# Performance work log

Hardware: AMD Instinct MI355X
Metric: run time of the kernel (lower is better)

## Reference

```python
import jax, jax.numpy as jnp
import numpy as np

B, NLEV, NX, NXSFC, NY, NYSFC, H, NHMEM = 4096, 60, 15, 24, 5, 5, 192, 16
G = 4 * H  # torch LSTM gate dim (i,f,g,o)


def setup_inputs() -> dict:
    key = jax.random.key(0)
    ks = jax.random.split(key, 32)
    rn = lambda k, s, sc=1.0: jax.random.normal(k, s, dtype=jnp.float32) * sc
    W = 0.05  # weight init scale for stability
    return {
        "x_lev": rn(ks[0], (B, NLEV, NX)),
        "x_sfc": rn(ks[1], (B, NXSFC)),
        "h_mem": jnp.zeros((B, NLEV, NHMEM), jnp.float32),
        "xmean_lev": rn(ks[2], (NLEV, NX), 0.1),
        "xdiv_lev": jax.random.uniform(ks[3], (NLEV, NX), dtype=jnp.float32) + 0.5,
        "xmean_sca": rn(ks[4], (NXSFC,), 0.1),
        "xdiv_sca": jax.random.uniform(ks[5], (NXSFC,), dtype=jnp.float32) + 0.5,
        "yscale_lev": jax.random.uniform(ks[6], (NLEV, NY), dtype=jnp.float32) + 0.5,
        "yscale_sca": jax.random.uniform(ks[7], (NY,), dtype=jnp.float32) + 0.5,
        "Wih1": rn(ks[8], (G, NX + NHMEM), W), "Whh1": rn(ks[9], (G, H), W), "b1": rn(ks[10], (G,), W),
        "Wih2": rn(ks[11], (G, H), W), "Whh2": rn(ks[12], (G, H), W), "b2": rn(ks[13], (G,), W),
        "Wsfc1": rn(ks[14], (H, NXSFC), W), "bsfc1": rn(ks[15], (H,), W),
        "Wsfc2": rn(ks[16], (H, NXSFC), W), "bsfc2": rn(ks[17], (H,), W),
        "Wtoa1": rn(ks[18], (H, 2), W), "btoa1": rn(ks[19], (H,), W),
        "Wtoa2": rn(ks[20], (H, 2), W), "btoa2": rn(ks[21], (H,), W),
        "Wlat": rn(ks[22], (NHMEM, H), W), "blat": rn(ks[23], (NHMEM,), W),
        "Wout": rn(ks[24], (NY, NHMEM), W), "bout": rn(ks[25], (NY,), W),
        "Wsfcout": rn(ks[26], (NY, H), W), "bsfcout": rn(ks[27], (NY,), W),
    }


def _lstm(x, h0, c0, Wih, Whh, b):
    """batch-first LSTM over the level dim. x: [B,L,nin]. Returns ([B,L,H], last h)."""
    xg = jnp.einsum('bli,gi->blg', x, Wih) + b  # precompute input projection
    def step(carry, xg_t):
        h, c = carry
        g = xg_t + h @ Whh.T
        i, f, gg, o = jnp.split(g, 4, axis=-1)  # torch gate order i,f,g,o
        c = jax.nn.sigmoid(f) * c + jax.nn.sigmoid(i) * jnp.tanh(gg)
        h = jax.nn.sigmoid(o) * jnp.tanh(c)
        return (h, c), h
    (hL, _), hs = jax.lax.scan(step, (h0, c0), jnp.swapaxes(xg, 0, 1))
    return jnp.swapaxes(hs, 0, 1), hL


def reference(x_lev, x_sfc, h_mem, xmean_lev, xdiv_lev, xmean_sca, xdiv_sca,
              yscale_lev, yscale_sca, Wih1, Whh1, b1, Wih2, Whh2, b2,
              Wsfc1, bsfc1, Wsfc2, bsfc2, Wtoa1, btoa1, Wtoa2, btoa2,
              Wlat, blat, Wout, bout, Wsfcout, bsfcout):
    # normalize
    xn = (x_lev - xmean_lev) / xdiv_lev                # [B,L,nx]
    sn = (x_sfc - xmean_sca) / xdiv_sca                # [B,nx_sfc]
    # surface MLPs initialize (h0, c0) of the upward LSTM
    h0 = jnp.tanh(sn @ Wsfc1.T + bsfc1)
    c0 = jnp.tanh(sn @ Wsfc2.T + bsfc2)
    # rnn1: concat latent memory to level inputs, scan surface -> TOA (flip levels)
    x1 = jnp.concatenate([xn, h_mem], axis=-1)[:, ::-1]
    hs1, _ = _lstm(x1, h0, c0, Wih1, Whh1, b1)
    hs1 = hs1[:, ::-1]                                  # back to TOA-first order
    # rnn2: TOA-initialized (2 solar scalars), scan TOA -> surface
    toa = sn[:, 0:2]
    h02 = jnp.tanh(toa @ Wtoa1.T + btoa1)
    c02 = jnp.tanh(toa @ Wtoa2.T + btoa2)
    hs2, h_last = _lstm(hs1, h02, c02, Wih2, Whh2, b2)
    # intermediate latent MLP -> new memory; output heads; denorm by yscale
    lat = hs2 @ Wlat.T + blat                           # [B,L,nh_mem]
    out = (lat @ Wout.T + bout) / yscale_lev            # [B,L,ny]
    out_sfc = (h_last @ Wsfcout.T + bsfcout) / yscale_sca  # [B,ny_sfc]
    return out, out_sfc, lat
```

## Files before the change

kernel.cpp:

```cpp
#include <hip/hip_runtime.h>
#include <hip/hip_bf16.h>


#define DEV static __device__ __forceinline__

typedef __attribute__((ext_vector_type(8))) short bf16x8;
typedef __attribute__((ext_vector_type(4))) float f32x4;

DEV unsigned short f2bf(float f) {
  unsigned int u = __builtin_bit_cast(unsigned int, f);
  unsigned int r = (u + 0x7fffu + ((u >> 16) & 1u)) >> 16;
  return (unsigned short)r;
}
DEV float bf2f(unsigned short s) {
  return __builtin_bit_cast(float, ((unsigned int)s) << 16);
}
DEV float sigm(float x) {
  float e = __builtin_amdgcn_exp2f(-1.44269504089f * x);
  return __builtin_amdgcn_rcpf(1.0f + e);
}
DEV float tanhf_(float x) {
  float e = __builtin_amdgcn_exp2f(2.88539008178f * x);
  return 1.0f - 2.0f * __builtin_amdgcn_rcpf(1.0f + e);
}

#define SEG_B2H 336
#define SEG_B2X 624
#define PACK_TOTAL (912 * 512)

#define HS1_OFF   1048576u
#define HS1_BYTES 94371840u
#define CWS_OFF   95420416u
#define CWS_BYTES 3145728u
#define XG2_OFF   98566144u
#define XG2_PER_LEVEL 12582912u
#define NEED_MIN  (HS1_OFF + HS1_BYTES)

__global__ void pack_kernel(const float* __restrict__ Wih1,
                            const float* __restrict__ Whh1,
                            const float* __restrict__ b1,
                            const float* __restrict__ Wih2,
                            const float* __restrict__ Whh2,
                            unsigned short* __restrict__ pw) {
  int idx = blockIdx.x * 256 + threadIdx.x;
  int j = idx & 7;
  int lane = (idx >> 3) & 63;
  int rest = idx >> 9;
  int n, k; float v;
  if (rest < SEG_B2H) {
    int kk = rest / 48, nt = rest % 48;
    n = nt * 16 + (lane & 15);
    k = kk * 32 + (lane >> 4) * 8 + j;
    if (k < 192) v = Whh1[n * 192 + k];
    else { int t = k - 192; v = (t < 31) ? Wih1[n * 31 + t] : b1[n]; }
  } else if (rest < SEG_B2X) {
    int r2 = rest - SEG_B2H; int kk = r2 / 48, nt = r2 % 48;
    n = nt * 16 + (lane & 15);
    k = kk * 32 + (lane >> 4) * 8 + j;
    v = Whh2[n * 192 + k];
  } else {
    int r2 = rest - SEG_B2X; int kk = r2 / 48, nt = r2 % 48;
    n = nt * 16 + (lane & 15);
    k = kk * 32 + (lane >> 4) * 8 + j;
    v = Wih2[n * 192 + k];
  }
  pw[idx] = f2bf(v);
}

__global__ __launch_bounds__(512, 2) void k1_lstm1(
    const float* __restrict__ xlev, const float* __restrict__ xsfc,
    const float* __restrict__ hmem,
    const float* __restrict__ xmean_lev, const float* __restrict__ xdiv_lev,
    const float* __restrict__ xmean_sca, const float* __restrict__ xdiv_sca,
    const float* __restrict__ Wsfc1, const float* __restrict__ bsfc1,
    const float* __restrict__ Wsfc2, const float* __restrict__ bsfc2,
    const unsigned short* __restrict__ pw,
    unsigned short* __restrict__ hs1g) {

  __shared__ float g_lds[16 * 772];
  __shared__ __align__(16) unsigned short a_lds[16 * 392];
  __shared__ float misc[16 * 24];

  const int tid = threadIdx.x;
  const int lane = tid & 63;
  const int wv = tid >> 6;
  const int bid = blockIdx.x;
  const int r0 = bid * 16;

  int erow[6], ecol[6];
  #pragma unroll
  for (int e = 0; e < 6; ++e) { int idx = tid + 512 * e; erow[e] = idx / 192; ecol[e] = idx % 192; }

  if (tid < 384) {
    int r = tid / 24, j = tid % 24;
    misc[tid] = (xsfc[(r0 + r) * 24 + j] - xmean_sca[j]) / xdiv_sca[j];
  }
  __syncthreads();

  float c[6];
  #pragma unroll
  for (int e = 0; e < 6; ++e) {
    int row = erow[e], col = ecol[e];
    float a1 = bsfc1[col], a2 = bsfc2[col];
    for (int k = 0; k < 24; ++k) {
      float s = misc[row * 24 + k];
      a1 = fmaf(s, Wsfc1[col * 24 + k], a1);
      a2 = fmaf(s, Wsfc2[col * 24 + k], a2);
    }
    a_lds[row * 392 + col] = f2bf(tanhf_(a1));
    c[e] = tanhf_(a2);
  }

  bf16x8 w1[7][6];
  #pragma unroll
  for (int kk = 0; kk < 7; ++kk)
    #pragma unroll
    for (int nt = 0; nt < 6; ++nt)
      w1[kk][nt] = *(const bf16x8*)&pw[((kk * 48 + wv * 6 + nt) * 64 + lane) * 8];

  const int xr = tid >> 5, xj = tid & 31;
  float xraw = 0.f;
  if (xj < 15)      xraw = __builtin_nontemporal_load(&xlev[((r0 + xr) * 60 + 59) * 15 + xj]);
  else if (xj < 31) xraw = __builtin_nontemporal_load(&hmem[((r0 + xr) * 60 + 59) * 16 + (xj - 15)]);

  for (int l = 59; l >= 0; --l) {
    {
      float v;
      if (xj < 15)      v = (xraw - xmean_lev[l * 15 + xj]) / xdiv_lev[l * 15 + xj];
      else if (xj < 31) v = xraw;
      else              v = 1.0f;
      a_lds[xr * 392 + 192 + xj] = f2bf(v);
    }
    if (l > 0) {
      if (xj < 15)      xraw = __builtin_nontemporal_load(&xlev[((r0 + xr) * 60 + l - 1) * 15 + xj]);
      else if (xj < 31) xraw = __builtin_nontemporal_load(&hmem[((r0 + xr) * 60 + l - 1) * 16 + (xj - 15)]);
    }
    __syncthreads();

    f32x4 acc[6];
    #pragma unroll
    for (int nt = 0; nt < 6; ++nt) acc[nt] = (f32x4){0.f, 0.f, 0.f, 0.f};
    #pragma unroll
    for (int kk = 0; kk < 7; ++kk) {
      const bf16x8 af = *(const bf16x8*)&a_lds[(lane & 15) * 392 + kk * 32 + (lane >> 4) * 8];
      #pragma unroll
      for (int nt = 0; nt < 6; ++nt)
        acc[nt] = __builtin_amdgcn_mfma_f32_16x16x32_bf16(af, w1[kk][nt], acc[nt], 0, 0, 0);
    }
    #pragma unroll
    for (int nt = 0; nt < 6; ++nt)
      #pragma unroll
      for (int q = 0; q < 4; ++q)
        g_lds[((lane >> 4) * 4 + q) * 772 + wv * 96 + nt * 16 + (lane & 15)] = acc[nt][q];
    __syncthreads();

    #pragma unroll
    for (int e = 0; e < 6; ++e) {
      int row = erow[e], col = ecol[e];
      float gi = g_lds[row * 772 + col];
      float gf = g_lds[row * 772 + 192 + col];
      float gg = g_lds[row * 772 + 384 + col];
      float go = g_lds[row * 772 + 576 + col];
      c[e] = sigm(gf) * c[e] + sigm(gi) * tanhf_(gg);
      float hv = sigm(go) * tanhf_(c[e]);
      unsigned short hb = f2bf(hv);
      a_lds[row * 392 + col] = hb;
      hs1g[(size_t)(bid * 60 + l) * 3072 + tid + 512 * e] = hb;
    }
  }
}

__global__ __launch_bounds__(512, 2) void k2_xg2(
    const unsigned short* __restrict__ pw,
    const unsigned short* __restrict__ hs1g,
    const float* __restrict__ b2,
    float* __restrict__ xg2, int l0, int Cc) {

  __shared__ __align__(16) unsigned short a2[8 * 16 * 200];

  const int tid = threadIdx.x;
  const int lane = tid & 63;
  const int wv = tid >> 6;
  const int g = blockIdx.x;

  bf16x8 wb[6][6];
  #pragma unroll
  for (int kk = 0; kk < 6; ++kk)
    #pragma unroll
    for (int nt = 0; nt < 6; ++nt)
      wb[kk][nt] = *(const bf16x8*)&pw[((SEG_B2X + kk * 48 + wv * 6 + nt) * 64 + lane) * 8];

  float b2v[6];
  #pragma unroll
  for (int nt = 0; nt < 6; ++nt) b2v[nt] = b2[wv * 96 + nt * 16 + (lane & 15)];

  #pragma unroll
  for (int i = 0; i < 6; ++i) {
    int flat16 = tid + 512 * i;
    int sub = flat16 / 384, within = flat16 % 384;
    int p2 = g * 8 + sub;
    int b3 = p2 / Cc, dl = p2 % Cc;
    bf16x8 v = *(const bf16x8*)&hs1g[(size_t)(b3 * 60 + l0 + dl) * 3072 + within * 8];
    int row = within / 24, col = (within % 24) * 8;
    *(bf16x8*)&a2[(sub * 16 + row) * 200 + col] = v;
  }
  __syncthreads();

  f32x4* xv = (f32x4*)xg2;
  for (int sub = 0; sub < 8; ++sub) {
    f32x4 acc[6];
    #pragma unroll
    for (int nt = 0; nt < 6; ++nt)
      acc[nt] = (f32x4){b2v[nt], b2v[nt], b2v[nt], b2v[nt]};
    #pragma unroll
    for (int kk = 0; kk < 6; ++kk) {
      const bf16x8 af = *(const bf16x8*)&a2[(sub * 16 + (lane & 15)) * 200 + kk * 32 + (lane >> 4) * 8];
      #pragma unroll
      for (int nt = 0; nt < 6; ++nt)
        acc[nt] = __builtin_amdgcn_mfma_f32_16x16x32_bf16(af, wb[kk][nt], acc[nt], 0, 0, 0);
    }
    int p2 = g * 8 + sub;
    #pragma unroll
    for (int nt = 0; nt < 6; ++nt)
      xv[(size_t)((p2 * 8 + wv) * 6 + nt) * 64 + lane] = acc[nt];
  }
}

__global__ __launch_bounds__(512, 2) void k3_lstm2(
    const float* __restrict__ xsfc,
    const float* __restrict__ xmean_sca, const float* __restrict__ xdiv_sca,
    const float* __restrict__ Wtoa1, const float* __restrict__ btoa1,
    const float* __restrict__ Wtoa2, const float* __restrict__ btoa2,
    const unsigned short* __restrict__ pw,
    const float* __restrict__ xg2,
    unsigned short* __restrict__ hs2,
    float* __restrict__ cws,
    int l0, int l1, int savec) {

  __shared__ float g_lds[16 * 772];
  __shared__ __align__(16) unsigned short a_lds[16 * 392];

  const int tid = threadIdx.x;
  const int lane = tid & 63;
  const int wv = tid >> 6;
  const int bid = blockIdx.x;
  const int r0 = bid * 16;
  const int Cc = l1 - l0;

  int erow[6], ecol[6];
  #pragma unroll
  for (int e = 0; e < 6; ++e) { int idx = tid + 512 * e; erow[e] = idx / 192; ecol[e] = idx % 192; }

  float c[6];
  if (l0 == 0) {
    #pragma unroll
    for (int e = 0; e < 6; ++e) {
      int row = erow[e], col = ecol[e];
      float t0 = (xsfc[(r0 + row) * 24 + 0] - xmean_sca[0]) / xdiv_sca[0];
      float t1 = (xsfc[(r0 + row) * 24 + 1] - xmean_sca[1]) / xdiv_sca[1];
      float a1 = fmaf(t0, Wtoa1[col * 2], fmaf(t1, Wtoa1[col * 2 + 1], btoa1[col]));
      float a2 = fmaf(t0, Wtoa2[col * 2], fmaf(t1, Wtoa2[col * 2 + 1], btoa2[col]));
      a_lds[row * 392 + col] = f2bf(tanhf_(a1));
      c[e] = tanhf_(a2);
    }
  } else {
    #pragma unroll
    for (int e = 0; e < 6; ++e) {
      a_lds[erow[e] * 392 + ecol[e]] = hs2[(size_t)(bid * 60 + (l0 - 1)) * 3072 + tid + 512 * e];
      c[e] = cws[bid * 3072 + tid + 512 * e];
    }
  }

  bf16x8 w2[6][6];
  #pragma unroll
  for (int kk = 0; kk < 6; ++kk)
    #pragma unroll
    for (int nt = 0; nt < 6; ++nt)
      w2[kk][nt] = *(const bf16x8*)&pw[((SEG_B2H + kk * 48 + wv * 6 + nt) * 64 + lane) * 8];

  const f32x4* xv = (const f32x4*)xg2;
  f32x4 cur[6];
  #pragma unroll
  for (int nt = 0; nt < 6; ++nt)
    cur[nt] = xv[(size_t)((bid * Cc + 0) * 8 + wv) * 6 * 64 + nt * 64 + lane];
  __syncthreads();

  for (int l = l0; l < l1; ++l) {
    f32x4 nxt[6];
    if (l + 1 < l1) {
      int p2n = bid * Cc + (l + 1 - l0);
      #pragma unroll
      for (int nt = 0; nt < 6; ++nt)
        nxt[nt] = xv[(size_t)(p2n * 8 + wv) * 6 * 64 + nt * 64 + lane];
    }

    f32x4 acc[6];
    #pragma unroll
    for (int nt = 0; nt < 6; ++nt) acc[nt] = cur[nt];
    #pragma unroll
    for (int kk = 0; kk < 6; ++kk) {
      const bf16x8 af = *(const bf16x8*)&a_lds[(lane & 15) * 392 + kk * 32 + (lane >> 4) * 8];
      #pragma unroll
      for (int nt = 0; nt < 6; ++nt)
        acc[nt] = __builtin_amdgcn_mfma_f32_16x16x32_bf16(af, w2[kk][nt], acc[nt], 0, 0, 0);
    }
    #pragma unroll
    for (int nt = 0; nt < 6; ++nt)
      #pragma unroll
      for (int q = 0; q < 4; ++q)
        g_lds[((lane >> 4) * 4 + q) * 772 + wv * 96 + nt * 16 + (lane & 15)] = acc[nt][q];
    __syncthreads();

    #pragma unroll
    for (int e = 0; e < 6; ++e) {
      int row = erow[e], col = ecol[e];
      float gi = g_lds[row * 772 + col];
      float gf = g_lds[row * 772 + 192 + col];
      float gg = g_lds[row * 772 + 384 + col];
      float go = g_lds[row * 772 + 576 + col];
      c[e] = sigm(gf) * c[e] + sigm(gi) * tanhf_(gg);
      unsigned short hb = f2bf(sigm(go) * tanhf_(c[e]));
      a_lds[row * 392 + col] = hb;
      hs2[(size_t)(bid * 60 + l) * 3072 + tid + 512 * e] = hb;
    }
    if (l + 1 < l1) {
      #pragma unroll
      for (int nt = 0; nt < 6; ++nt) cur[nt] = nxt[nt];
    }
    __syncthreads();
  }

  if (savec) {
    #pragma unroll
    for (int e = 0; e < 6; ++e)
      cws[bid * 3072 + tid + 512 * e] = c[e];
  }
}

__global__ __launch_bounds__(256, 4) void k4_out(
    const unsigned short* __restrict__ hs2,
    const float* __restrict__ Wlat, const float* __restrict__ blat,
    const float* __restrict__ Wout, const float* __restrict__ bout,
    const float* __restrict__ Wsfcout, const float* __restrict__ bsfcout,
    const float* __restrict__ yscale_lev, const float* __restrict__ yscale_sca,
    float* __restrict__ out, float* __restrict__ outsfc, float* __restrict__ latout) {

  __shared__ float wl[16 * 192];
  const int tid = threadIdx.x;
  const int bid = blockIdx.x;

  if (bid < 960) {
    for (int i = tid; i < 3072; i += 256) wl[i] = Wlat[i];
    __syncthreads();
    int R = bid * 256 + tid;
    int b = R / 60, l = R % 60, b3 = b >> 4, r = b & 15;
    const unsigned short* hp = hs2 + (size_t)(b3 * 60 + l) * 3072 + r * 192;
    float lat[16];
    #pragma unroll
    for (int cc = 0; cc < 16; ++cc) lat[cc] = blat[cc];
    for (int k8 = 0; k8 < 24; ++k8) {
      bf16x8 hv = *(const bf16x8*)&hp[k8 * 8];
      #pragma unroll
      for (int j = 0; j < 8; ++j) {
        float hf = bf2f((unsigned short)hv[j]);
        #pragma unroll
        for (int cc = 0; cc < 16; ++cc) lat[cc] = fmaf(hf, wl[cc * 192 + k8 * 8 + j], lat[cc]);
      }
    }
    #pragma unroll
    for (int cc = 0; cc < 16; ++cc)
      latout[(size_t)R * 16 + cc] = lat[cc];
    #pragma unroll
    for (int y = 0; y < 5; ++y) {
      float ov = bout[y];
      #pragma unroll
      for (int cc = 0; cc < 16; ++cc) ov = fmaf(lat[cc], Wout[y * 16 + cc], ov);
      out[(size_t)R * 5 + y] = ov / yscale_lev[l * 5 + y];
    }
  } else {
    for (int i = tid; i < 960; i += 256) wl[i] = Wsfcout[i];
    __syncthreads();
    int r = (bid - 960) * 256 + tid;
    int b3 = r >> 4, rr = r & 15;
    const unsigned short* hp = hs2 + (size_t)(b3 * 60 + 59) * 3072 + rr * 192;
    float a5[5];
    #pragma unroll
    for (int y = 0; y < 5; ++y) a5[y] = bsfcout[y];
    for (int k8 = 0; k8 < 24; ++k8) {
      bf16x8 hv = *(const bf16x8*)&hp[k8 * 8];
      #pragma unroll
      for (int j = 0; j < 8; ++j) {
        float hf = bf2f((unsigned short)hv[j]);
        #pragma unroll
        for (int y = 0; y < 5; ++y) a5[y] = fmaf(hf, wl[y * 192 + k8 * 8 + j], a5[y]);
      }
    }
    #pragma unroll
    for (int y = 0; y < 5; ++y)
      outsfc[(size_t)r * 5 + y] = a5[y] / yscale_sca[y];
  }
}

__global__ __launch_bounds__(512, 2) void lstm_main(
    const float* __restrict__ xlev, const float* __restrict__ xsfc,
    const float* __restrict__ hmem,
    const float* __restrict__ xmean_lev, const float* __restrict__ xdiv_lev,
    const float* __restrict__ xmean_sca, const float* __restrict__ xdiv_sca,
    const float* __restrict__ yscale_lev, const float* __restrict__ yscale_sca,
    const float* __restrict__ b2,
    const float* __restrict__ Wsfc1, const float* __restrict__ bsfc1,
    const float* __restrict__ Wsfc2, const float* __restrict__ bsfc2,
    const float* __restrict__ Wtoa1, const float* __restrict__ btoa1,
    const float* __restrict__ Wtoa2, const float* __restrict__ btoa2,
    const float* __restrict__ Wlat, const float* __restrict__ blat,
    const float* __restrict__ Wout, const float* __restrict__ bout,
    const float* __restrict__ Wsfcout, const float* __restrict__ bsfcout,
    const unsigned short* __restrict__ pw,
    unsigned short* __restrict__ hs1g,
    float* __restrict__ out, float* __restrict__ outsfc, float* __restrict__ latout) {

  __shared__ float g_lds[16 * 772];
  __shared__ __align__(16) unsigned short a_lds[16 * 392];
  __shared__ float misc[16 * 24];
  __shared__ float toa_lds[32];

  const int tid = threadIdx.x;
  const int lane = tid & 63;
  const int wv = tid >> 6;
  const int bid = blockIdx.x;
  const int r0 = bid * 16;

  int erow[6], ecol[6];
  #pragma unroll
  for (int e = 0; e < 6; ++e) { int idx = tid + 512 * e; erow[e] = idx / 192; ecol[e] = idx % 192; }

  if (tid < 384) {
    int r = tid / 24, j = tid % 24;
    misc[tid] = (xsfc[(r0 + r) * 24 + j] - xmean_sca[j]) / xdiv_sca[j];
  }
  __syncthreads();
  if (tid < 32) toa_lds[tid] = misc[(tid >> 1) * 24 + (tid & 1)];

  float c[6];
  #pragma unroll
  for (int e = 0; e < 6; ++e) {
    int row = erow[e], col = ecol[e];
    float a1 = bsfc1[col], a2 = bsfc2[col];
    for (int k = 0; k < 24; ++k) {
      float s = misc[row * 24 + k];
      a1 = fmaf(s, Wsfc1[col * 24 + k], a1);
      a2 = fmaf(s, Wsfc2[col * 24 + k], a2);
    }
    a_lds[row * 392 + col] = f2bf(tanhf_(a1));
    c[e] = tanhf_(a2);
  }

  bf16x8 w1[7][6];
  #pragma unroll
  for (int kk = 0; kk < 7; ++kk)
    #pragma unroll
    for (int nt = 0; nt < 6; ++nt)
      w1[kk][nt] = *(const bf16x8*)&pw[((kk * 48 + wv * 6 + nt) * 64 + lane) * 8];

  const int xr = tid >> 5, xj = tid & 31;
  float xraw = 0.f;
  if (xj < 15)      xraw = __builtin_nontemporal_load(&xlev[((r0 + xr) * 60 + 59) * 15 + xj]);
  else if (xj < 31) xraw = __builtin_nontemporal_load(&hmem[((r0 + xr) * 60 + 59) * 16 + (xj - 15)]);

  for (int l = 59; l >= 0; --l) {
    {
      float v;
      if (xj < 15)      v = (xraw - xmean_lev[l * 15 + xj]) / xdiv_lev[l * 15 + xj];
      else if (xj < 31) v = xraw;
      else              v = 1.0f;
      a_lds[xr * 392 + 192 + xj] = f2bf(v);
    }
    if (l > 0) {
      if (xj < 15)      xraw = __builtin_nontemporal_load(&xlev[((r0 + xr) * 60 + l - 1) * 15 + xj]);
      else if (xj < 31) xraw = __builtin_nontemporal_load(&hmem[((r0 + xr) * 60 + l - 1) * 16 + (xj - 15)]);
    }
    __syncthreads();

    f32x4 acc[6];
    #pragma unroll
    for (int nt = 0; nt < 6; ++nt) acc[nt] = (f32x4){0.f, 0.f, 0.f, 0.f};
    #pragma unroll
    for (int kk = 0; kk < 7; ++kk) {
      const bf16x8 af = *(const bf16x8*)&a_lds[(lane & 15) * 392 + kk * 32 + (lane >> 4) * 8];
      #pragma unroll
      for (int nt = 0; nt < 6; ++nt)
        acc[nt] = __builtin_amdgcn_mfma_f32_16x16x32_bf16(af, w1[kk][nt], acc[nt], 0, 0, 0);
    }
    #pragma unroll
    for (int nt = 0; nt < 6; ++nt)
      #pragma unroll
      for (int q = 0; q < 4; ++q)
        g_lds[((lane >> 4) * 4 + q) * 772 + wv * 96 + nt * 16 + (lane & 15)] = acc[nt][q];
    __syncthreads();

    #pragma unroll
    for (int e = 0; e < 6; ++e) {
      int row = erow[e], col = ecol[e];
      float gi = g_lds[row * 772 + col];
      float gf = g_lds[row * 772 + 192 + col];
      float gg = g_lds[row * 772 + 384 + col];
      float go = g_lds[row * 772 + 576 + col];
      c[e] = sigm(gf) * c[e] + sigm(gi) * tanhf_(gg);
      float hv = sigm(go) * tanhf_(c[e]);
      unsigned short hb = f2bf(hv);
      a_lds[row * 392 + col] = hb;
      __builtin_nontemporal_store(hb, &hs1g[(bid * 60 + l) * 3072 + tid + 512 * e]);
    }
  }

  #pragma unroll
  for (int e = 0; e < 6; ++e) {
    int row = erow[e], col = ecol[e];
    float t0 = toa_lds[row * 2], t1 = toa_lds[row * 2 + 1];
    float a1 = fmaf(t0, Wtoa1[col * 2], fmaf(t1, Wtoa1[col * 2 + 1], btoa1[col]));
    float a2 = fmaf(t0, Wtoa2[col * 2], fmaf(t1, Wtoa2[col * 2 + 1], btoa2[col]));
    a_lds[row * 392 + col] = f2bf(tanhf_(a1));
    c[e] = tanhf_(a2);
  }
  bf16x8 w2[6][6];
  #pragma unroll
  for (int kk = 0; kk < 6; ++kk)
    #pragma unroll
    for (int nt = 0; nt < 6; ++nt)
      w2[kk][nt] = *(const bf16x8*)&pw[((SEG_B2H + kk * 48 + wv * 6 + nt) * 64 + lane) * 8];

  const bf16x8* hs1v = (const bf16x8*)hs1g;
  bf16x8 hv8;
  if (tid < 384) hv8 = __builtin_nontemporal_load(&hs1v[(bid * 60 + 0) * 384 + tid]);

  for (int l = 0; l < 60; ++l) {
    if (tid < 384)
      *(bf16x8*)&a_lds[(tid / 24) * 392 + 192 + (tid % 24) * 8] = hv8;
    if (tid < 384 && l < 59)
      hv8 = __builtin_nontemporal_load(&hs1v[(bid * 60 + l + 1) * 384 + tid]);

    bf16x8 wx0[6], wx1[6];
    #pragma unroll
    for (int nt = 0; nt < 6; ++nt)
      wx0[nt] = *(const bf16x8*)&pw[((SEG_B2X + 0 * 48 + wv * 6 + nt) * 64 + lane) * 8];
    #pragma unroll
    for (int nt = 0; nt < 6; ++nt)
      wx1[nt] = *(const bf16x8*)&pw[((SEG_B2X + 1 * 48 + wv * 6 + nt) * 64 + lane) * 8];

    __syncthreads();

    f32x4 acc[6];
    #pragma unroll
    for (int nt = 0; nt < 6; ++nt) acc[nt] = (f32x4){0.f, 0.f, 0.f, 0.f};

    #pragma unroll
    for (int g = 0; g < 6; ++g) {
      const bf16x8 ah = *(const bf16x8*)&a_lds[(lane & 15) * 392 + g * 32 + (lane >> 4) * 8];
      #pragma unroll
      for (int nt = 0; nt < 6; ++nt)
        acc[nt] = __builtin_amdgcn_mfma_f32_16x16x32_bf16(ah, w2[g][nt], acc[nt], 0, 0, 0);
      const bf16x8 ax = *(const bf16x8*)&a_lds[(lane & 15) * 392 + 192 + g * 32 + (lane >> 4) * 8];
      #pragma unroll
      for (int nt = 0; nt < 6; ++nt)
        acc[nt] = __builtin_amdgcn_mfma_f32_16x16x32_bf16(ax, (g & 1) ? wx1[nt] : wx0[nt], acc[nt], 0, 0, 0);
      if (g < 4) {
        #pragma unroll
        for (int nt = 0; nt < 6; ++nt) {
          bf16x8 nw = *(const bf16x8*)&pw[((SEG_B2X + (g + 2) * 48 + wv * 6 + nt) * 64 + lane) * 8];
          if (g & 1) wx1[nt] = nw; else wx0[nt] = nw;
        }
      }
    }
    #pragma unroll
    for (int nt = 0; nt < 6; ++nt)
      #pragma unroll
      for (int q = 0; q < 4; ++q)
        g_lds[((lane >> 4) * 4 + q) * 772 + wv * 96 + nt * 16 + (lane & 15)] = acc[nt][q];
    __syncthreads();

    #pragma unroll
    for (int e = 0; e < 6; ++e) {
      int row = erow[e], col = ecol[e];
      float gi = g_lds[row * 772 + col]       + b2[col];
      float gf = g_lds[row * 772 + 192 + col] + b2[192 + col];
      float gg = g_lds[row * 772 + 384 + col] + b2[384 + col];
      float go = g_lds[row * 772 + 576 + col] + b2[576 + col];
      c[e] = sigm(gf) * c[e] + sigm(gi) * tanhf_(gg);
      a_lds[row * 392 + col] = f2bf(sigm(go) * tanhf_(c[e]));
    }
    __syncthreads();

    if (tid < 256) {
      int r = tid >> 4, cc = tid & 15;
      float lv = blat[cc];
      for (int k = 0; k < 192; k += 8) {
        #pragma unroll
        for (int jj = 0; jj < 8; ++jj)
          lv = fmaf(bf2f(a_lds[r * 392 + k + jj]), Wlat[cc * 192 + k + jj], lv);
      }
      __builtin_nontemporal_store(lv, &latout[((r0 + r) * 60 + l) * 16 + cc]);
      misc[r * 16 + cc] = lv;
    }
    __syncthreads();
    if (tid < 80) {
      int r = tid / 5, y = tid % 5;
      float ov = bout[y];
      #pragma unroll
      for (int k = 0; k < 16; ++k) ov = fmaf(misc[r * 16 + k], Wout[y * 16 + k], ov);
      __builtin_nontemporal_store(ov / yscale_lev[l * 5 + y], &out[((r0 + r) * 60 + l) * 5 + y]);
    }
  }

  if (tid < 80) {
    int r = tid / 5, y = tid % 5;
    float ov = bsfcout[y];
    for (int k = 0; k < 192; ++k)
      ov = fmaf(bf2f(a_lds[r * 392 + k]), Wsfcout[y * 192 + k], ov);
    outsfc[(r0 + r) * 5 + y] = ov / yscale_sca[y];
  }
}

extern "C" void kernel_launch(void* const* d_in, const int* in_sizes, int n_in,
                              void* d_out, int out_size, void* d_ws, size_t ws_size,
                              hipStream_t stream) {
  (void)in_sizes; (void)n_in; (void)out_size;

  const float* xlev      = (const float*)d_in[0];
  const float* xsfc      = (const float*)d_in[1];
  const float* hmem      = (const float*)d_in[2];
  const float* xmean_lev = (const float*)d_in[3];
  const float* xdiv_lev  = (const float*)d_in[4];
  const float* xmean_sca = (const float*)d_in[5];
  const float* xdiv_sca  = (const float*)d_in[6];
  const float* yscale_lev= (const float*)d_in[7];
  const float* yscale_sca= (const float*)d_in[8];
  const float* Wih1      = (const float*)d_in[9];
  const float* Whh1      = (const float*)d_in[10];
  const float* b1        = (const float*)d_in[11];
  const float* Wih2      = (const float*)d_in[12];
  const float* Whh2      = (const float*)d_in[13];
  const float* b2        = (const float*)d_in[14];
  const float* Wsfc1     = (const float*)d_in[15];
  const float* bsfc1     = (const float*)d_in[16];
  const float* Wsfc2     = (const float*)d_in[17];
  const float* bsfc2     = (const float*)d_in[18];
  const float* Wtoa1     = (const float*)d_in[19];
  const float* btoa1     = (const float*)d_in[20];
  const float* Wtoa2     = (const float*)d_in[21];
  const float* btoa2     = (const float*)d_in[22];
  const float* Wlat      = (const float*)d_in[23];
  const float* blat      = (const float*)d_in[24];
  const float* Wout      = (const float*)d_in[25];
  const float* bout      = (const float*)d_in[26];
  const float* Wsfcout   = (const float*)d_in[27];
  const float* bsfcout   = (const float*)d_in[28];

  unsigned short* pw   = (unsigned short*)d_ws;
  unsigned short* hsg  = (unsigned short*)((char*)d_ws + HS1_OFF);
  float* cws           = (float*)((char*)d_ws + CWS_OFF);
  float* xg2           = (float*)((char*)d_ws + XG2_OFF);
  float* out    = (float*)d_out;
  float* outsfc = out + (size_t)4096 * 60 * 5;
  float* latout = outsfc + (size_t)4096 * 5;

  long long avail = (long long)ws_size - (long long)XG2_OFF;
  int C = (avail > 0) ? (int)(avail / (long long)XG2_PER_LEVEL) : 0;
  if (C > 60) C = 60;

  hipLaunchKernelGGL(pack_kernel, dim3(PACK_TOTAL / 256), dim3(256), 0, stream,
                     Wih1, Whh1, b1, Wih2, Whh2, pw);

  if (C >= 1) {
    hipLaunchKernelGGL(k1_lstm1, dim3(256), dim3(512), 0, stream,
                       xlev, xsfc, hmem, xmean_lev, xdiv_lev, xmean_sca, xdiv_sca,
                       Wsfc1, bsfc1, Wsfc2, bsfc2, pw, hsg);
    int l0 = 0;
    while (l0 < 60) {
      int Cc = (60 - l0 < C) ? (60 - l0) : C;
      hipLaunchKernelGGL(k2_xg2, dim3(32 * Cc), dim3(512), 0, stream,
                         pw, hsg, b2, xg2, l0, Cc);
      hipLaunchKernelGGL(k3_lstm2, dim3(256), dim3(512), 0, stream,
                         xsfc, xmean_sca, xdiv_sca, Wtoa1, btoa1, Wtoa2, btoa2,
                         pw, xg2, hsg, cws, l0, l0 + Cc, (l0 + Cc < 60) ? 1 : 0);
      l0 += Cc;
    }
    hipLaunchKernelGGL(k4_out, dim3(976), dim3(256), 0, stream,
                       hsg, Wlat, blat, Wout, bout, Wsfcout, bsfcout,
                       yscale_lev, yscale_sca, out, outsfc, latout);
  } else if (ws_size >= (size_t)NEED_MIN) {
    hipLaunchKernelGGL(lstm_main, dim3(256), dim3(512), 0, stream,
                       xlev, xsfc, hmem, xmean_lev, xdiv_lev, xmean_sca, xdiv_sca,
                       yscale_lev, yscale_sca, b2,
                       Wsfc1, bsfc1, Wsfc2, bsfc2, Wtoa1, btoa1, Wtoa2, btoa2,
                       Wlat, blat, Wout, bout, Wsfcout, bsfcout,
                       pw, hsg, out, outsfc, latout);
  }
}
```

Measured before the change: 777.8 us.

## Fuse both LSTM scans and the Wih2 projection into one persistent kernel

Merges the LSTM1 scan, the chunked LSTM2 input projection and the LSTM2 scan into a single templated kernel launched once per batch tile. Each block computes its own chunk of `xg2` with MFMA, writes it to global memory, then runs the recurrent steps for that chunk, so the cell state stays in registers between chunks. This removes the per-chunk launches and the c-state save and restore through memory. In exchange, the projection now runs serially inside the 256 recurrent blocks instead of on a wider grid. The larger shared-memory footprint and the `accG[CC][6]` register array risk lower occupancy and register spills.

```diff
diff --git a/kernel.cpp b/kernel.cpp
--- a/kernel.cpp
+++ b/kernel.cpp
@@ -28,13 +28,11 @@
 #define SEG_B2X 624
 #define PACK_TOTAL (912 * 512)
 
-#define HS1_OFF   1048576u
-#define HS1_BYTES 94371840u
-#define CWS_OFF   95420416u
-#define CWS_BYTES 3145728u
-#define XG2_OFF   98566144u
+#define HS_OFF    1048576u
+#define HS_BYTES  94371840u
+#define XG2_OFF   95420416u
 #define XG2_PER_LEVEL 12582912u
-#define NEED_MIN  (HS1_OFF + HS1_BYTES)
+#define NEED_MIN  (HS_OFF + HS_BYTES)
 
 __global__ void pack_kernel(const float* __restrict__ Wih1,
                             const float* __restrict__ Whh1,
@@ -67,18 +65,24 @@
   pw[idx] = f2bf(v);
 }
 
-__global__ __launch_bounds__(512, 2) void k1_lstm1(
+template <int CC>
+__global__ __launch_bounds__(512, 2) void mono(
     const float* __restrict__ xlev, const float* __restrict__ xsfc,
     const float* __restrict__ hmem,
     const float* __restrict__ xmean_lev, const float* __restrict__ xdiv_lev,
     const float* __restrict__ xmean_sca, const float* __restrict__ xdiv_sca,
     const float* __restrict__ Wsfc1, const float* __restrict__ bsfc1,
     const float* __restrict__ Wsfc2, const float* __restrict__ bsfc2,
+    const float* __restrict__ Wtoa1, const float* __restrict__ btoa1,
+    const float* __restrict__ Wtoa2, const float* __restrict__ btoa2,
+    const float* __restrict__ b2,
     const unsigned short* __restrict__ pw,
-    unsigned short* __restrict__ hs1g) {
+    unsigned short* __restrict__ hsg,
+    float* __restrict__ xg2) {
 
   __shared__ float g_lds[16 * 772];
   __shared__ __align__(16) unsigned short a_lds[16 * 392];
+  __shared__ __align__(16) unsigned short a2[CC * 16 * 200];
   __shared__ float misc[16 * 24];
 
   const int tid = threadIdx.x;
@@ -101,239 +105,197 @@
   #pragma unroll
   for (int e = 0; e < 6; ++e) {
     int row = erow[e], col = ecol[e];
-    float a1 = bsfc1[col], a2 = bsfc2[col];
+    float a1 = bsfc1[col], a2v = bsfc2[col];
     for (int k = 0; k < 24; ++k) {
       float s = misc[row * 24 + k];
-      a1 = fmaf(s, Wsfc1[col * 24 + k], a1);
-      a2 = fmaf(s, Wsfc2[col * 24 + k], a2);
+      a1  = fmaf(s, Wsfc1[col * 24 + k], a1);
+      a2v = fmaf(s, Wsfc2[col * 24 + k], a2v);
     }
     a_lds[row * 392 + col] = f2bf(tanhf_(a1));
-    c[e] = tanhf_(a2);
-  }
-
-  bf16x8 w1[7][6];
-  #pragma unroll
-  for (int kk = 0; kk < 7; ++kk)
-    #pragma unroll
-    for (int nt = 0; nt < 6; ++nt)
-      w1[kk][nt] = *(const bf16x8*)&pw[((kk * 48 + wv * 6 + nt) * 64 + lane) * 8];
-
-  const int xr = tid >> 5, xj = tid & 31;
-  float xraw = 0.f;
-  if (xj < 15)      xraw = __builtin_nontemporal_load(&xlev[((r0 + xr) * 60 + 59) * 15 + xj]);
-  else if (xj < 31) xraw = __builtin_nontemporal_load(&hmem[((r0 + xr) * 60 + 59) * 16 + (xj - 15)]);
-
-  for (int l = 59; l >= 0; --l) {
+    c[e] = tanhf_(a2v);
+  }
+
+  {
+    bf16x8 w1[7][6];
+    #pragma unroll
+    for (int kk = 0; kk < 7; ++kk)
+      #pragma unroll
+      for (int nt = 0; nt < 6; ++nt)
+        w1[kk][nt] = *(const bf16x8*)&pw[((kk * 48 + wv * 6 + nt) * 64 + lane) * 8];
+
+    const int xr = tid >> 5, xj = tid & 31;
+    float xraw = 0.f;
+    if (xj < 15)      xraw = __builtin_nontemporal_load(&xlev[((r0 + xr) * 60 + 59) * 15 + xj]);
+    else if (xj < 31) xraw = __builtin_nontemporal_load(&hmem[((r0 + xr) * 60 + 59) * 16 + (xj - 15)]);
+
+    for (int l = 59; l >= 0; --l) {
+      {
+        float v;
+        if (xj < 15)      v = (xraw - xmean_lev[l * 15 + xj]) / xdiv_lev[l * 15 + xj];
+        else if (xj < 31) v = xraw;
+        else              v = 1.0f;
+        a_lds[xr * 392 + 192 + xj] = f2bf(v);
+      }
+      if (l > 0) {
+        if (xj < 15)      xraw = __builtin_nontemporal_load(&xlev[((r0 + xr) * 60 + l - 1) * 15 + xj]);
+        else if (xj < 31) xraw = __builtin_nontemporal_load(&hmem[((r0 + xr) * 60 + l - 1) * 16 + (xj - 15)]);
+      }
+      __syncthreads();
+
+      f32x4 acc[6];
+      #pragma unroll
+      for (int nt = 0; nt < 6; ++nt) acc[nt] = (f32x4){0.f, 0.f, 0.f, 0.f};
+      #pragma unroll
+      for (int kk = 0; kk < 7; ++kk) {
+        const bf16x8 af = *(const bf16x8*)&a_lds[(lane & 15) * 392 + kk * 32 + (lane >> 4) * 8];
+        #pragma unroll
+        for (int nt = 0; nt < 6; ++nt)
+          acc[nt] = __builtin_amdgcn_mfma_f32_16x16x32_bf16(af, w1[kk][nt], acc[nt], 0, 0, 0);
+      }
+      #pragma unroll
+      for (int nt = 0; nt < 6; ++nt)
+        #pragma unroll
+        for (int q = 0; q < 4; ++q)
+          g_lds[((lane >> 4) * 4 + q) * 772 + wv * 96 + nt * 16 + (lane & 15)] = acc[nt][q];
+      __syncthreads();
+
+      #pragma unroll
+      for (int e = 0; e < 6; ++e) {
+        int row = erow[e], col = ecol[e];
+        float gi = g_lds[row * 772 + col];
+        float gf = g_lds[row * 772 + 192 + col];
+        float gg = g_lds[row * 772 + 384 + col];
+        float go = g_lds[row * 772 + 576 + col];
+        c[e] = sigm(gf) * c[e] + sigm(gi) * tanhf_(gg);
+        float hv = sigm(go) * tanhf_(c[e]);
+        unsigned short hb = f2bf(hv);
+        a_lds[row * 392 + col] = hb;
+        hsg[(size_t)(bid * 60 + l) * 3072 + tid + 512 * e] = hb;
+      }
+    }
+  }
+
+  #pragma unroll
+  for (int e = 0; e < 6; ++e) {
+    int row = erow[e], col = ecol[e];
+    float t0 = (xsfc[(r0 + row) * 24 + 0] - xmean_sca[0]) / xdiv_sca[0];
+    float t1 = (xsfc[(r0 + row) * 24 + 1] - xmean_sca[1]) / xdiv_sca[1];
+    float a1 = fmaf(t0, Wtoa1[col * 2], fmaf(t1, Wtoa1[col * 2 + 1], btoa1[col]));
+    float a2v = fmaf(t0, Wtoa2[col * 2], fmaf(t1, Wtoa2[col * 2 + 1], btoa2[col]));
+    a_lds[row * 392 + col] = f2bf(tanhf_(a1));
+    c[e] = tanhf_(a2v);
+  }
+
+  float b2v[6];
+  #pragma unroll
+  for (int nt = 0; nt < 6; ++nt) b2v[nt] = b2[wv * 96 + nt * 16 + (lane & 15)];
+
+  f32x4* xv = (f32x4*)xg2;
+
+  for (int l0 = 0; l0 < 60; l0 += CC) {
+    __syncthreads();
+
+    #pragma unroll
+    for (int i = 0; i < (384 * CC + 511) / 512; ++i) {
+      int idx = tid + 512 * i;
+      if (idx < 384 * CC) {
+        int dl = idx / 384, within = idx % 384;
+        bf16x8 v = *(const bf16x8*)&hsg[(size_t)(bid * 60 + l0 + dl) * 3072 + within * 8];
+        *(bf16x8*)&a2[(dl * 16 + within / 24) * 200 + (within % 24) * 8] = v;
+      }
+    }
+    __syncthreads();
+
     {
-      float v;
-      if (xj < 15)      v = (xraw - xmean_lev[l * 15 + xj]) / xdiv_lev[l * 15 + xj];
-      else if (xj < 31) v = xraw;
-      else              v = 1.0f;
-      a_lds[xr * 392 + 192 + xj] = f2bf(v);
-    }
-    if (l > 0) {
-      if (xj < 15)      xraw = __builtin_nontemporal_load(&xlev[((r0 + xr) * 60 + l - 1) * 15 + xj]);
-      else if (xj < 31) xraw = __builtin_nontemporal_load(&hmem[((r0 + xr) * 60 + l - 1) * 16 + (xj - 15)]);
-    }
-    __syncthreads();
-
-    f32x4 acc[6];
-    #pragma unroll
-    for (int nt = 0; nt < 6; ++nt) acc[nt] = (f32x4){0.f, 0.f, 0.f, 0.f};
-    #pragma unroll
-    for (int kk = 0; kk < 7; ++kk) {
-      const bf16x8 af = *(const bf16x8*)&a_lds[(lane & 15) * 392 + kk * 32 + (lane >> 4) * 8];
-      #pragma unroll
-      for (int nt = 0; nt < 6; ++nt)
-        acc[nt] = __builtin_amdgcn_mfma_f32_16x16x32_bf16(af, w1[kk][nt], acc[nt], 0, 0, 0);
-    }
-    #pragma unroll
-    for (int nt = 0; nt < 6; ++nt)
-      #pragma unroll
-      for (int q = 0; q < 4; ++q)
-        g_lds[((lane >> 4) * 4 + q) * 772 + wv * 96 + nt * 16 + (lane & 15)] = acc[nt][q];
-    __syncthreads();
-
-    #pragma unroll
-    for (int e = 0; e < 6; ++e) {
-      int row = erow[e], col = ecol[e];
-      float gi = g_lds[row * 772 + col];
-      float gf = g_lds[row * 772 + 192 + col];
-      float gg = g_lds[row * 772 + 384 + col];
-      float go = g_lds[row * 772 + 576 + col];
-      c[e] = sigm(gf) * c[e] + sigm(gi) * tanhf_(gg);
-      float hv = sigm(go) * tanhf_(c[e]);
-      unsigned short hb = f2bf(hv);
-      a_lds[row * 392 + col] = hb;
-      hs1g[(size_t)(bid * 60 + l) * 3072 + tid + 512 * e] = hb;
-    }
-  }
-}
-
-__global__ __launch_bounds__(512, 2) void k2_xg2(
-    const unsigned short* __restrict__ pw,
-    const unsigned short* __restrict__ hs1g,
-    const float* __restrict__ b2,
-    float* __restrict__ xg2, int l0, int Cc) {
-
-  __shared__ __align__(16) unsigned short a2[8 * 16 * 200];
-
-  const int tid = threadIdx.x;
-  const int lane = tid & 63;
-  const int wv = tid >> 6;
-  const int g = blockIdx.x;
-
-  bf16x8 wb[6][6];
-  #pragma unroll
-  for (int kk = 0; kk < 6; ++kk)
-    #pragma unroll
-    for (int nt = 0; nt < 6; ++nt)
-      wb[kk][nt] = *(const bf16x8*)&pw[((SEG_B2X + kk * 48 + wv * 6 + nt) * 64 + lane) * 8];
-
-  float b2v[6];
-  #pragma unroll
-  for (int nt = 0; nt < 6; ++nt) b2v[nt] = b2[wv * 96 + nt * 16 + (lane & 15)];
-
-  #pragma unroll
-  for (int i = 0; i < 6; ++i) {
-    int flat16 = tid + 512 * i;
-    int sub = flat16 / 384, within = flat16 % 384;
-    int p2 = g * 8 + sub;
-    int b3 = p2 / Cc, dl = p2 % Cc;
-    bf16x8 v = *(const bf16x8*)&hs1g[(size_t)(b3 * 60 + l0 + dl) * 3072 + within * 8];
-    int row = within / 24, col = (within % 24) * 8;
-    *(bf16x8*)&a2[(sub * 16 + row) * 200 + col] = v;
-  }
-  __syncthreads();
-
-  f32x4* xv = (f32x4*)xg2;
-  for (int sub = 0; sub < 8; ++sub) {
-    f32x4 acc[6];
-    #pragma unroll
-    for (int nt = 0; nt < 6; ++nt)
-      acc[nt] = (f32x4){b2v[nt], b2v[nt], b2v[nt], b2v[nt]};
-    #pragma unroll
-    for (int kk = 0; kk < 6; ++kk) {
-      const bf16x8 af = *(const bf16x8*)&a2[(sub * 16 + (lane & 15)) * 200 + kk * 32 + (lane >> 4) * 8];
-      #pragma unroll
-      for (int nt = 0; nt < 6; ++nt)
-        acc[nt] = __builtin_amdgcn_mfma_f32_16x16x32_bf16(af, wb[kk][nt], acc[nt], 0, 0, 0);
-    }
-    int p2 = g * 8 + sub;
-    #pragma unroll
-    for (int nt = 0; nt < 6; ++nt)
-      xv[(size_t)((p2 * 8 + wv) * 6 + nt) * 64 + lane] = acc[nt];
-  }
-}
-
-__global__ __launch_bounds__(512, 2) void k3_lstm2(
-    const float* __restrict__ xsfc,
-    const float* __restrict__ xmean_sca, const float* __restrict__ xdiv_sca,
-    const float* __restrict__ Wtoa1, const float* __restrict__ btoa1,
-    const float* __restrict__ Wtoa2, const float* __restrict__ btoa2,
-    const unsigned short* __restrict__ pw,
-    const float* __restrict__ xg2,
-    unsigned short* __restrict__ hs2,
-    float* __restrict__ cws,
-    int l0, int l1, int savec) {
-
-  __shared__ float g_lds[16 * 772];
-  __shared__ __align__(16) unsigned short a_lds[16 * 392];
-
-  const int tid = threadIdx.x;
-  const int lane = tid & 63;
-  const int wv = tid >> 6;
-  const int bid = blockIdx.x;
-  const int r0 = bid * 16;
-  const int Cc = l1 - l0;
-
-  int erow[6], ecol[6];
-  #pragma unroll
-  for (int e = 0; e < 6; ++e) { int idx = tid + 512 * e; erow[e] = idx / 192; ecol[e] = idx % 192; }
-
-  float c[6];
-  if (l0 == 0) {
-    #pragma unroll
-    for (int e = 0; e < 6; ++e) {
-      int row = erow[e], col = ecol[e];
-      float t0 = (xsfc[(r0 + row) * 24 + 0] - xmean_sca[0]) / xdiv_sca[0];
-      float t1 = (xsfc[(r0 + row) * 24 + 1] - xmean_sca[1]) / xdiv_sca[1];
-      float a1 = fmaf(t0, Wtoa1[col * 2], fmaf(t1, Wtoa1[col * 2 + 1], btoa1[col]));
-      float a2 = fmaf(t0, Wtoa2[col * 2], fmaf(t1, Wtoa2[col * 2 + 1], btoa2[col]));
-      a_lds[row * 392 + col] = f2bf(tanhf_(a1));
-      c[e] = tanhf_(a2);
-    }
-  } else {
-    #pragma unroll
-    for (int e = 0; e < 6; ++e) {
-      a_lds[erow[e] * 392 + ecol[e]] = hs2[(size_t)(bid * 60 + (l0 - 1)) * 3072 + tid + 512 * e];
-      c[e] = cws[bid * 3072 + tid + 512 * e];
-    }
-  }
-
-  bf16x8 w2[6][6];
-  #pragma unroll
-  for (int kk = 0; kk < 6; ++kk)
-    #pragma unroll
-    for (int nt = 0; nt < 6; ++nt)
-      w2[kk][nt] = *(const bf16x8*)&pw[((SEG_B2H + kk * 48 + wv * 6 + nt) * 64 + lane) * 8];
-
-  const f32x4* xv = (const f32x4*)xg2;
-  f32x4 cur[6];
-  #pragma unroll
-  for (int nt = 0; nt < 6; ++nt)
-    cur[nt] = xv[(size_t)((bid * Cc + 0) * 8 + wv) * 6 * 64 + nt * 64 + lane];
-  __syncthreads();
-
-  for (int l = l0; l < l1; ++l) {
-    f32x4 nxt[6];
-    if (l + 1 < l1) {
-      int p2n = bid * Cc + (l + 1 - l0);
-      #pragma unroll
-      for (int nt = 0; nt < 6; ++nt)
-        nxt[nt] = xv[(size_t)(p2n * 8 + wv) * 6 * 64 + nt * 64 + lane];
-    }
-
-    f32x4 acc[6];
-    #pragma unroll
-    for (int nt = 0; nt < 6; ++nt) acc[nt] = cur[nt];
-    #pragma unroll
-    for (int kk = 0; kk < 6; ++kk) {
-      const bf16x8 af = *(const bf16x8*)&a_lds[(lane & 15) * 392 + kk * 32 + (lane >> 4) * 8];
-      #pragma unroll
-      for (int nt = 0; nt < 6; ++nt)
-        acc[nt] = __builtin_amdgcn_mfma_f32_16x16x32_bf16(af, w2[kk][nt], acc[nt], 0, 0, 0);
-    }
-    #pragma unroll
-    for (int nt = 0; nt < 6; ++nt)
-      #pragma unroll
-      for (int q = 0; q < 4; ++q)
-        g_lds[((lane >> 4) * 4 + q) * 772 + wv * 96 + nt * 16 + (lane & 15)] = acc[nt][q];
-    __syncthreads();
-
-    #pragma unroll
-    for (int e = 0; e < 6; ++e) {
-      int row = erow[e], col = ecol[e];
-      float gi = g_lds[row * 772 + col];
-      float gf = g_lds[row * 772 + 192 + col];
-      float gg = g_lds[row * 772 + 384 + col];
-      float go = g_lds[row * 772 + 576 + col];
-      c[e] = sigm(gf) * c[e] + sigm(gi) * tanhf_(gg);
-      unsigned short hb = f2bf(sigm(go) * tanhf_(c[e]));
-      a_lds[row * 392 + col] = hb;
-      hs2[(size_t)(bid * 60 + l) * 3072 + tid + 512 * e] = hb;
-    }
-    if (l + 1 < l1) {
-      #pragma unroll
-      for (int nt = 0; nt < 6; ++nt) cur[nt] = nxt[nt];
-    }
-    __syncthreads();
-  }
-
-  if (savec) {
-    #pragma unroll
-    for (int e = 0; e < 6; ++e)
-      cws[bid * 3072 + tid + 512 * e] = c[e];
+      f32x4 accG[CC][6];
+      #pragma unroll
+      for (int dl = 0; dl < CC; ++dl)
+        #pragma unroll
+        for (int nt = 0; nt < 6; ++nt)
+          accG[dl][nt] = (f32x4){b2v[nt], b2v[nt], b2v[nt], b2v[nt]};
+
+      bf16x8 wxA[6], wxB[6];
+      #pragma unroll
+      for (int nt = 0; nt < 6; ++nt)
+        wxA[nt] = *(const bf16x8*)&pw[((SEG_B2X + 0 * 48 + wv * 6 + nt) * 64 + lane) * 8];
+      #pragma unroll
+      for (int nt = 0; nt < 6; ++nt)
+        wxB[nt] = *(const bf16x8*)&pw[((SEG_B2X + 1 * 48 + wv * 6 + nt) * 64 + lane) * 8];
+
+      #pragma unroll
+      for (int kk = 0; kk < 6; ++kk) {
+        #pragma unroll
+        for (int dl = 0; dl < CC; ++dl) {
+          const bf16x8 af = *(const bf16x8*)&a2[(dl * 16 + (lane & 15)) * 200 + kk * 32 + (lane >> 4) * 8];
+          #pragma unroll
+          for (int nt = 0; nt < 6; ++nt)
+            accG[dl][nt] = __builtin_amdgcn_mfma_f32_16x16x32_bf16(
+                af, (kk & 1) ? wxB[nt] : wxA[nt], accG[dl][nt], 0, 0, 0);
+        }
+        if (kk < 4) {
+          #pragma unroll
+          for (int nt = 0; nt < 6; ++nt) {
+            bf16x8 nw = *(const bf16x8*)&pw[((SEG_B2X + (kk + 2) * 48 + wv * 6 + nt) * 64 + lane) * 8];
+            if (kk & 1) wxB[nt] = nw; else wxA[nt] = nw;
+          }
+        }
+      }
+
+      #pragma unroll
+      for (int dl = 0; dl < CC; ++dl)
+        #pragma unroll
+        for (int nt = 0; nt < 6; ++nt)
+          xv[(size_t)(((bid * CC + dl) * 8 + wv) * 6 + nt) * 64 + lane] = accG[dl][nt];
+    }
+    __syncthreads();
+
+    bf16x8 w2[6][6];
+    #pragma unroll
+    for (int kk = 0; kk < 6; ++kk)
+      #pragma unroll
+      for (int nt = 0; nt < 6; ++nt)
+        w2[kk][nt] = *(const bf16x8*)&pw[((SEG_B2H + kk * 48 + wv * 6 + nt) * 64 + lane) * 8];
+
+    #pragma unroll
+    for (int dl = 0; dl < CC; ++dl) {
+      const int l = l0 + dl;
+      f32x4 cur[6];
+      #pragma unroll
+      for (int nt = 0; nt < 6; ++nt)
+        cur[nt] = xv[(size_t)(((bid * CC + dl) * 8 + wv) * 6 + nt) * 64 + lane];
+
+      f32x4 acc[6];
+      #pragma unroll
+      for (int nt = 0; nt < 6; ++nt) acc[nt] = (f32x4){0.f, 0.f, 0.f, 0.f};
+      #pragma unroll
+      for (int kk = 0; kk < 6; ++kk) {
+        const bf16x8 af = *(const bf16x8*)&a_lds[(lane & 15) * 392 + kk * 32 + (lane >> 4) * 8];
+        #pragma unroll
+        for (int nt = 0; nt < 6; ++nt)
+          acc[nt] = __builtin_amdgcn_mfma_f32_16x16x32_bf16(af, w2[kk][nt], acc[nt], 0, 0, 0);
+      }
+      #pragma unroll
+      for (int nt = 0; nt < 6; ++nt)
+        #pragma unroll
+        for (int q = 0; q < 4; ++q)
+          g_lds[((lane >> 4) * 4 + q) * 772 + wv * 96 + nt * 16 + (lane & 15)] =
+              acc[nt][q] + cur[nt][q];
+      __syncthreads();
+
+      #pragma unroll
+      for (int e = 0; e < 6; ++e) {
+        int row = erow[e], col = ecol[e];
+        float gi = g_lds[row * 772 + col];
+        float gf = g_lds[row * 772 + 192 + col];
+        float gg = g_lds[row * 772 + 384 + col];
+        float go = g_lds[row * 772 + 576 + col];
+        c[e] = sigm(gf) * c[e] + sigm(gi) * tanhf_(gg);
+        unsigned short hb = f2bf(sigm(go) * tanhf_(c[e]));
+        a_lds[row * 392 + col] = hb;
+        hsg[(size_t)(bid * 60 + l) * 3072 + tid + 512 * e] = hb;
+      }
+      __syncthreads();
+    }
   }
 }
 
@@ -655,35 +617,31 @@
   const float* Wsfcout   = (const float*)d_in[27];
   const float* bsfcout   = (const float*)d_in[28];
 
-  unsigned short* pw   = (unsigned short*)d_ws;
-  unsigned short* hsg  = (unsigned short*)((char*)d_ws + HS1_OFF);
-  float* cws           = (float*)((char*)d_ws + CWS_OFF);
-  float* xg2           = (float*)((char*)d_ws + XG2_OFF);
+  unsigned short* pw  = (unsigned short*)d_ws;
+  unsigned short* hsg = (unsigned short*)((char*)d_ws + HS_OFF);
+  float* xg2          = (float*)((char*)d_ws + XG2_OFF);
   float* out    = (float*)d_out;
   float* outsfc = out + (size_t)4096 * 60 * 5;
   float* latout = outsfc + (size_t)4096 * 5;
 
-  long long avail = (long long)ws_size - (long long)XG2_OFF;
-  int C = (avail > 0) ? (int)(avail / (long long)XG2_PER_LEVEL) : 0;
-  if (C > 60) C = 60;
-
   hipLaunchKernelGGL(pack_kernel, dim3(PACK_TOTAL / 256), dim3(256), 0, stream,
                      Wih1, Whh1, b1, Wih2, Whh2, pw);
 
-  if (C >= 1) {
-    hipLaunchKernelGGL(k1_lstm1, dim3(256), dim3(512), 0, stream,
-                       xlev, xsfc, hmem, xmean_lev, xdiv_lev, xmean_sca, xdiv_sca,
-                       Wsfc1, bsfc1, Wsfc2, bsfc2, pw, hsg);
-    int l0 = 0;
-    while (l0 < 60) {
-      int Cc = (60 - l0 < C) ? (60 - l0) : C;
-      hipLaunchKernelGGL(k2_xg2, dim3(32 * Cc), dim3(512), 0, stream,
-                         pw, hsg, b2, xg2, l0, Cc);
-      hipLaunchKernelGGL(k3_lstm2, dim3(256), dim3(512), 0, stream,
-                         xsfc, xmean_sca, xdiv_sca, Wtoa1, btoa1, Wtoa2, btoa2,
-                         pw, xg2, hsg, cws, l0, l0 + Cc, (l0 + Cc < 60) ? 1 : 0);
-      l0 += Cc;
-    }
+  const size_t need6 = (size_t)XG2_OFF + 6ull * XG2_PER_LEVEL;
+  const size_t need3 = (size_t)XG2_OFF + 3ull * XG2_PER_LEVEL;
+  const size_t need1 = (size_t)XG2_OFF + 1ull * XG2_PER_LEVEL;
+
+  if (ws_size >= need1) {
+    #define MONO_ARGS xlev, xsfc, hmem, xmean_lev, xdiv_lev, xmean_sca, xdiv_sca, \
+                      Wsfc1, bsfc1, Wsfc2, bsfc2, Wtoa1, btoa1, Wtoa2, btoa2, b2, \
+                      pw, hsg, xg2
+    if (ws_size >= need6)
+      hipLaunchKernelGGL(mono<6>, dim3(256), dim3(512), 0, stream, MONO_ARGS);
+    else if (ws_size >= need3)
+      hipLaunchKernelGGL(mono<3>, dim3(256), dim3(512), 0, stream, MONO_ARGS);
+    else
+      hipLaunchKernelGGL(mono<1>, dim3(256), dim3(512), 0, stream, MONO_ARGS);
+    #undef MONO_ARGS
     hipLaunchKernelGGL(k4_out, dim3(976), dim3(256), 0, stream,
                        hsg, Wlat, blat, Wout, bout, Wsfcout, bsfcout,
                        yscale_lev, yscale_sca, out, outsfc, latout);
```

Result: slower. 1.275 ms (+64.0%).

## Use lighter LDS-only barriers, shrink xg2 tiles and add xg2 after MFMA

Applied to the files above, without the earlier changes.

Replaces __syncthreads with a custom barrier that waits only on LDS/scalar counters (lgkmcnt) before s_barrier, so outstanding global prefetch loads no longer stall each recurrence step. The xg2 projection kernel now does 2 sub-tiles per block instead of 8, with four times as many blocks, which cuts LDS use and adds parallelism at the cost of reloading the weight registers more often. In lstm2 the prefetched input projection is added at the LDS store instead of seeding the MFMA accumulator, which frees the MFMA chain from waiting on the global load. The custom barrier relies on global loads not being needed before the barrier, which holds only if no global writes are read across it.

```diff
diff --git a/kernel.cpp b/kernel.cpp
--- a/kernel.cpp
+++ b/kernel.cpp
@@ -23,18 +23,20 @@
   float e = __builtin_amdgcn_exp2f(2.88539008178f * x);
   return 1.0f - 2.0f * __builtin_amdgcn_rcpf(1.0f + e);
 }
+DEV void sbar() {
+  asm volatile("s_waitcnt lgkmcnt(0)\n\ts_barrier" ::: "memory");
+}
 
 #define SEG_B2H 336
 #define SEG_B2X 624
 #define PACK_TOTAL (912 * 512)
 
-#define HS1_OFF   1048576u
-#define HS1_BYTES 94371840u
+#define HS_OFF    1048576u
+#define HS_BYTES  94371840u
 #define CWS_OFF   95420416u
-#define CWS_BYTES 3145728u
 #define XG2_OFF   98566144u
 #define XG2_PER_LEVEL 12582912u
-#define NEED_MIN  (HS1_OFF + HS1_BYTES)
+#define NEED_MIN  (HS_OFF + HS_BYTES)
 
 __global__ void pack_kernel(const float* __restrict__ Wih1,
                             const float* __restrict__ Whh1,
@@ -135,7 +137,7 @@
       if (xj < 15)      xraw = __builtin_nontemporal_load(&xlev[((r0 + xr) * 60 + l - 1) * 15 + xj]);
       else if (xj < 31) xraw = __builtin_nontemporal_load(&hmem[((r0 + xr) * 60 + l - 1) * 16 + (xj - 15)]);
     }
-    __syncthreads();
+    sbar();
 
     f32x4 acc[6];
     #pragma unroll
@@ -152,7 +154,7 @@
       #pragma unroll
       for (int q = 0; q < 4; ++q)
         g_lds[((lane >> 4) * 4 + q) * 772 + wv * 96 + nt * 16 + (lane & 15)] = acc[nt][q];
-    __syncthreads();
+    sbar();
 
     #pragma unroll
     for (int e = 0; e < 6; ++e) {
@@ -176,7 +178,7 @@
     const float* __restrict__ b2,
     float* __restrict__ xg2, int l0, int Cc) {
 
-  __shared__ __align__(16) unsigned short a2[8 * 16 * 200];
+  __shared__ __align__(16) unsigned short a2[2 * 16 * 200];
 
   const int tid = threadIdx.x;
   const int lane = tid & 63;
@@ -195,19 +197,21 @@
   for (int nt = 0; nt < 6; ++nt) b2v[nt] = b2[wv * 96 + nt * 16 + (lane & 15)];
 
   #pragma unroll
-  for (int i = 0; i < 6; ++i) {
+  for (int i = 0; i < 2; ++i) {
     int flat16 = tid + 512 * i;
-    int sub = flat16 / 384, within = flat16 % 384;
-    int p2 = g * 8 + sub;
-    int b3 = p2 / Cc, dl = p2 % Cc;
-    bf16x8 v = *(const bf16x8*)&hs1g[(size_t)(b3 * 60 + l0 + dl) * 3072 + within * 8];
-    int row = within / 24, col = (within % 24) * 8;
-    *(bf16x8*)&a2[(sub * 16 + row) * 200 + col] = v;
-  }
-  __syncthreads();
+    if (flat16 < 768) {
+      int sub = flat16 / 384, within = flat16 % 384;
+      int p2 = g * 2 + sub;
+      int b3 = p2 / Cc, dl = p2 % Cc;
+      bf16x8 v = *(const bf16x8*)&hs1g[(size_t)(b3 * 60 + l0 + dl) * 3072 + within * 8];
+      *(bf16x8*)&a2[(sub * 16 + within / 24) * 200 + (within % 24) * 8] = v;
+    }
+  }
+  sbar();
 
   f32x4* xv = (f32x4*)xg2;
-  for (int sub = 0; sub < 8; ++sub) {
+  #pragma unroll
+  for (int sub = 0; sub < 2; ++sub) {
     f32x4 acc[6];
     #pragma unroll
     for (int nt = 0; nt < 6; ++nt)
@@ -219,7 +223,7 @@
       for (int nt = 0; nt < 6; ++nt)
         acc[nt] = __builtin_amdgcn_mfma_f32_16x16x32_bf16(af, wb[kk][nt], acc[nt], 0, 0, 0);
     }
-    int p2 = g * 8 + sub;
+    int p2 = g * 2 + sub;
     #pragma unroll
     for (int nt = 0; nt < 6; ++nt)
       xv[(size_t)((p2 * 8 + wv) * 6 + nt) * 64 + lane] = acc[nt];
@@ -296,7 +300,7 @@
 
     f32x4 acc[6];
     #pragma unroll
-    for (int nt = 0; nt < 6; ++nt) acc[nt] = cur[nt];
+    for (int nt = 0; nt < 6; ++nt) acc[nt] = (f32x4){0.f, 0.f, 0.f, 0.f};
     #pragma unroll
     for (int kk = 0; kk < 6; ++kk) {
       const bf16x8 af = *(const bf16x8*)&a_lds[(lane & 15) * 392 + kk * 32 + (lane >> 4) * 8];
@@ -308,8 +312,9 @@
     for (int nt = 0; nt < 6; ++nt)
       #pragma unroll
       for (int q = 0; q < 4; ++q)
-        g_lds[((lane >> 4) * 4 + q) * 772 + wv * 96 + nt * 16 + (lane & 15)] = acc[nt][q];
-    __syncthreads();
+        g_lds[((lane >> 4) * 4 + q) * 772 + wv * 96 + nt * 16 + (lane & 15)] =
+            acc[nt][q] + cur[nt][q];
+    sbar();
 
     #pragma unroll
     for (int e = 0; e < 6; ++e) {
@@ -327,7 +332,7 @@
       #pragma unroll
       for (int nt = 0; nt < 6; ++nt) cur[nt] = nxt[nt];
     }
-    __syncthreads();
+    sbar();
   }
 
   if (savec) {
@@ -655,10 +660,10 @@
   const float* Wsfcout   = (const float*)d_in[27];
   const float* bsfcout   = (const float*)d_in[28];
 
-  unsigned short* pw   = (unsigned short*)d_ws;
-  unsigned short* hsg  = (unsigned short*)((char*)d_ws + HS1_OFF);
-  float* cws           = (float*)((char*)d_ws + CWS_OFF);
-  float* xg2           = (float*)((char*)d_ws + XG2_OFF);
+  unsigned short* pw  = (unsigned short*)d_ws;
+  unsigned short* hsg = (unsigned short*)((char*)d_ws + HS_OFF);
+  float* cws          = (float*)((char*)d_ws + CWS_OFF);
+  float* xg2          = (float*)((char*)d_ws + XG2_OFF);
   float* out    = (float*)d_out;
   float* outsfc = out + (size_t)4096 * 60 * 5;
   float* latout = outsfc + (size_t)4096 * 5;
@@ -677,7 +682,7 @@
     int l0 = 0;
     while (l0 < 60) {
       int Cc = (60 - l0 < C) ? (60 - l0) : C;
-      hipLaunchKernelGGL(k2_xg2, dim3(32 * Cc), dim3(512), 0, stream,
+      hipLaunchKernelGGL(k2_xg2, dim3(128 * Cc), dim3(512), 0, stream,
                          pw, hsg, b2, xg2, l0, Cc);
       hipLaunchKernelGGL(k3_lstm2, dim3(256), dim3(512), 0, stream,
                          xsfc, xmean_sca, xdiv_sca, Wtoa1, btoa1, Wtoa2, btoa2,
```

After: 816.2 us. +4.9%, slower.
